# Kernel tuning notes

Measured on AMD Instinct MI355X. Metric: run time of the kernel, lower is better.

The kernel has to match this reference:

```python
import jax, jax.numpy as jnp
import numpy as np

EMBED = 50
SEQ = 100
NLABEL = 15
HID = 20
VOCAB = 50000
BATCH = 8192


def gru_scan(xs, W, U, b, return_sequences):
    """Keras GRUCell (reset_after=True, gate order z,r,h).
    xs: (B, T, D). W: (D, 3H), U: (H, 3H), b: (2, 3H) [input bias, recurrent bias].
    """
    B = xs.shape[0]
    H = U.shape[0]
    bi, br = b[0], b[1]
    h0 = jnp.zeros((B, H), dtype=xs.dtype)

    def step(h, x_t):
        mx = x_t @ W + bi                      # (B, 3H)
        mh = h @ U + br                        # (B, 3H)
        xz, xr, xh = mx[:, :H], mx[:, H:2*H], mx[:, 2*H:]
        hz, hr, hh_ = mh[:, :H], mh[:, H:2*H], mh[:, 2*H:]
        z = jax.nn.sigmoid(xz + hz)
        r = jax.nn.sigmoid(xr + hr)
        hh = jnp.tanh(xh + r * hh_)
        h_new = z * h + (1.0 - z) * hh
        return h_new, h_new

    xs_t = jnp.swapaxes(xs, 0, 1)              # (T, B, D)
    h_last, hs = jax.lax.scan(step, h0, xs_t)
    if return_sequences:
        return jnp.swapaxes(hs, 0, 1)          # (B, T, H)
    return h_last                               # (B, H)


def setup_inputs() -> dict:
    key = jax.random.key(0)
    ks = jax.random.split(key, 9)
    s = 0.05
    return {
        "x": jax.random.randint(ks[0], (BATCH, SEQ), 0, VOCAB),
        "emb_table": jax.random.normal(ks[1], (VOCAB, EMBED), jnp.float32) * s,
        "W1": jax.random.normal(ks[2], (EMBED, 3 * HID), jnp.float32) * s,
        "U1": jax.random.normal(ks[3], (HID, 3 * HID), jnp.float32) * s,
        "b1": jnp.zeros((2, 3 * HID), jnp.float32),
        "W2": jax.random.normal(ks[4], (HID, 3 * HID), jnp.float32) * s,
        "U2": jax.random.normal(ks[5], (HID, 3 * HID), jnp.float32) * s,
        "b2": jnp.zeros((2, 3 * HID), jnp.float32),
        "Wd": jax.random.normal(ks[6], (HID, NLABEL), jnp.float32) * s,
        "bd": jnp.zeros((NLABEL,), jnp.float32),
        "drop_rate": 0,
    }


def reference(x, emb_table, W1, U1, b1, W2, U2, b2, Wd, bd, drop_rate):
    emb = emb_table[x]                               # (B, T, E)
    seq = gru_scan(emb, W1, U1, b1, return_sequences=True)   # (B, T, H)
    enc = gru_scan(seq, W2, U2, b2, return_sequences=False)  # (B, H)
    # drop_rate == 0 -> tf.nn.dropout is identity
    logits = enc @ Wd + bd                           # (B, 15)
    return logits
```

## Files before the change

kernel.cpp:

```cpp
#include <hip/hip_runtime.h>
#include <hip/hip_bf16.h>
#include <hip/hip_fp16.h>

#define SEQ_T 100
#define HID 20
#define EMB_D 50
#define VOCAB_N 50000
#define TABW 60
#define NTILE 3125
#define BBLK 782

typedef short sh8 __attribute__((ext_vector_type(8)));
typedef float f4  __attribute__((ext_vector_type(4)));

#define OFF_U1P 0
#define OFF_W2P 600
#define OFF_U2P 1200
#define OFF_B1  3600
#define OFF_B2  3720
#define OFF_WD  3840
#define OFF_BD  4140
#define OFF_TAB 4160

__device__ __forceinline__ float ldf(const void* p, int i, int isf) {
  return isf ? ((const float*)p)[i]
             : __bfloat162float(((const __hip_bfloat16*)p)[i]);
}
__device__ __forceinline__ short f2bf(float f) {
  unsigned u = __float_as_uint(f);
  u += 0x7fffu + ((u >> 16) & 1u);
  return (short)(u >> 16);
}
__device__ __forceinline__ float rdl(float v, int l) {
  return __uint_as_float(__builtin_amdgcn_readlane(__float_as_uint(v), l));
}
__device__ __forceinline__ int detect_isf(const void* emb) {
  uint4 dv = ((const uint4*)emb)[threadIdx.x & 63];
  int big = 0;
#pragma unroll
  for (int i = 0; i < 4; ++i) {
    unsigned w = ((const unsigned*)&dv)[i];
    big |= (((w >> 7) & 0xFF) >= 140) | (((w >> 23) & 0xFF) >= 140);
  }
  return (__ballot(big) != 0ull) ? 1 : 0;
}

__global__ __launch_bounds__(256) void build_table(
    const void* __restrict__ emb, const void* __restrict__ W1,
    const void* __restrict__ b1,
    const void* __restrict__ U1, const void* __restrict__ W2,
    const void* __restrict__ U2, const void* __restrict__ b2,
    const void* __restrict__ Wd, const void* __restrict__ bd,
    float* __restrict__ ws)
{
  const int isf = detect_isf(emb);
  if (blockIdx.x == 0) {
    const int t = threadIdx.x;
    unsigned* wsu = (unsigned*)ws;
    for (int i = t; i < 600; i += 256) {
      const int j = i / 10, p = i % 10;
      const int k0 = 2 * p, k1 = 2 * p + 1;
#define PK(M) ((unsigned)__half_as_ushort(__float2half_rn(ldf(M, k0 * 60 + j, isf))) | \
               ((unsigned)__half_as_ushort(__float2half_rn(ldf(M, k1 * 60 + j, isf))) << 16))
      wsu[OFF_U1P + i] = PK(U1);
      wsu[OFF_W2P + i] = PK(W2);
      wsu[OFF_U2P + i] = PK(U2);
#undef PK
    }
    for (int i = t; i < 120; i += 256) {
      ws[OFF_B1 + i] = ldf(b1, i, isf);
      ws[OFF_B2 + i] = ldf(b2, i, isf);
    }
    for (int i = t; i < 300; i += 256) ws[OFF_WD + i] = ldf(Wd, i, isf);
    for (int i = t; i < 15;  i += 256) ws[OFF_BD + i] = ldf(bd, i, isf);
  }

  const int L = threadIdx.x & 63, q = L >> 4, c = L & 15;
  const int wid = blockIdx.x * 4 + (threadIdx.x >> 6);
  float* __restrict__ tab = ws + OFF_TAB;

  __shared__ int4 sB[64][8];
  if (threadIdx.x < 64) {
#pragma unroll
    for (int nt = 0; nt < 4; ++nt) {
      const int col = nt * 16 + c;
      sh8 B0, B1;
#pragma unroll
      for (int jj = 0; jj < 8; ++jj) {
        const int k0 = q * 8 + jj, k1 = 32 + q * 8 + jj;
        B0[jj] = (col < TABW) ? f2bf(ldf(W1, k0 * TABW + col, isf)) : (short)0;
        B1[jj] = (col < TABW && k1 < EMB_D)
                     ? f2bf(ldf(W1, k1 * TABW + col, isf)) : (short)0;
      }
      sB[L][nt * 2]     = *(const int4*)&B0;
      sB[L][nt * 2 + 1] = *(const int4*)&B1;
    }
  }
  float bi[4];
#pragma unroll
  for (int nt = 0; nt < 4; ++nt) {
    const int col = nt * 16 + c;
    bi[nt] = (col < TABW) ? ldf(b1, col, isf) : 0.f;
  }
  __syncthreads();

  for (int tile = wid; tile < NTILE; tile += BBLK * 4) {
    const int v0 = tile * 16;
    sh8 A0, A1;
#pragma unroll
    for (int jj = 0; jj < 8; ++jj) { A0[jj] = 0; A1[jj] = 0; }
    if (!isf) {
      const unsigned short* eb = (const unsigned short*)emb;
      const size_t rb = (size_t)(v0 + c) * EMB_D;
#pragma unroll
      for (int i = 0; i < 4; ++i) {
        unsigned d = *(const unsigned*)(eb + rb + q * 8 + 2 * i);
        A0[2 * i] = (short)(d & 0xffff); A0[2 * i + 1] = (short)(d >> 16);
      }
      const int k1b = 32 + q * 8;
#pragma unroll
      for (int i = 0; i < 4; ++i) {
        const int k = k1b + 2 * i;
        if (k + 1 < EMB_D) {
          unsigned d = *(const unsigned*)(eb + rb + k);
          A1[2 * i] = (short)(d & 0xffff); A1[2 * i + 1] = (short)(d >> 16);
        }
      }
    } else {
      const float* ef = (const float*)emb;
      const size_t rb = (size_t)(v0 + c) * EMB_D;
#pragma unroll
      for (int jj = 0; jj < 8; ++jj) {
        const int k0 = q * 8 + jj, k1 = 32 + q * 8 + jj;
        A0[jj] = f2bf(ef[rb + k0]);
        A1[jj] = (k1 < EMB_D) ? f2bf(ef[rb + k1]) : (short)0;
      }
    }
#pragma unroll
    for (int nt = 0; nt < 4; ++nt) {
      int4 b0i = sB[L][nt * 2], b1i = sB[L][nt * 2 + 1];
      sh8 B0 = *(const sh8*)&b0i, B1 = *(const sh8*)&b1i;
      const int col = nt * 16 + c;
      f4 acc = { bi[nt], bi[nt], bi[nt], bi[nt] };
      acc = __builtin_amdgcn_mfma_f32_16x16x32_bf16(A0, B0, acc, 0, 0, 0);
      acc = __builtin_amdgcn_mfma_f32_16x16x32_bf16(A1, B1, acc, 0, 0, 0);
      if (col < TABW) {
#pragma unroll
        for (int r = 0; r < 4; ++r)
          tab[(size_t)(v0 + q * 4 + r) * TABW + col] = acc[r];
      }
    }
  }
}

__global__ __launch_bounds__(256, 8) void gru_main(
    const int* __restrict__ x, const float* __restrict__ ws,
    const void* __restrict__ emb, void* __restrict__ out)
{
  const int isf = detect_isf(emb);
  const int j = threadIdx.x & 63;
  const int e = __builtin_amdgcn_readfirstlane(blockIdx.x * 4 + (threadIdx.x >> 6));
  const int jc = j < TABW ? j : 0;

  const int* xr = x + (size_t)e * SEQ_T;
  const float* tab = ws + OFF_TAB;
  const int o1 = jc * 40;
  const int jc4 = jc * 4;
  const int a1 = ((j - 20) & 63) * 4;
  const int a2 = ((j + 40) & 63) * 4;
  const float br1 = ws[OFF_B1 + 60 + jc];
  const float bi2 = ws[OFF_B2 + jc];
  const float br2 = ws[OFF_B2 + 60 + jc];
  float h2out;

  asm volatile(
    "global_load_dwordx4 v[10:13], %[o1], %[wsp] offset:0\n\t"
    "global_load_dwordx4 v[14:17], %[o1], %[wsp] offset:16\n\t"
    "global_load_dwordx2 v[18:19], %[o1], %[wsp] offset:32\n\t"
    "v_add_u32 v44, 0x960, %[o1]\n\t"
    "v_add_u32 v45, 0x12c0, %[o1]\n\t"
    "global_load_dwordx4 v[20:23], v44, %[wsp] offset:0\n\t"
    "global_load_dwordx4 v[24:27], v44, %[wsp] offset:16\n\t"
    "global_load_dwordx2 v[28:29], v44, %[wsp] offset:32\n\t"
    "global_load_dwordx4 v[30:33], v45, %[wsp] offset:0\n\t"
    "global_load_dwordx4 v[34:37], v45, %[wsp] offset:16\n\t"
    "global_load_dwordx2 v[38:39], v45, %[wsp] offset:32\n\t"
    "s_mov_b64 s[20:21], 0\n\ts_mov_b64 s[22:23], 0\n\t"
    "s_mov_b64 s[24:25], 0\n\ts_mov_b64 s[26:27], 0\n\t"
    "s_mov_b64 s[28:29], 0\n\t"
    "s_mov_b64 s[30:31], 0\n\ts_mov_b64 s[32:33], 0\n\t"
    "s_mov_b64 s[34:35], 0\n\ts_mov_b64 s[36:37], 0\n\t"
    "s_mov_b64 s[38:39], 0\n\t"
    "s_mov_b64 s[40:41], 0\n\ts_mov_b64 s[42:43], 0\n\t"
    "s_mov_b64 s[44:45], 0\n\ts_mov_b64 s[46:47], 0\n\t"
    "s_mov_b64 s[48:49], 0\n\t"
    "s_mov_b64 s[50:51], 0\n\ts_mov_b64 s[52:53], 0\n\t"
    "s_mov_b64 s[54:55], 0\n\ts_mov_b64 s[56:57], 0\n\t"
    "s_mov_b64 s[58:59], 0\n\t"
    "v_mov_b32 v40, 0\n\t"
    "v_mov_b32 v41, 0\n\t"
    "s_load_dword s65, %[xp], 0x0\n\t"
    "s_load_dword s66, %[xp], 0x4\n\t"
    "s_load_dword s68, %[xp], 0x8\n\t"
    "s_waitcnt lgkmcnt(0)\n\t"
    "s_mul_i32 s65, s65, 240\n\t"
    "s_mul_i32 s66, s66, 240\n\t"
    "s_mul_i32 s68, s68, 240\n\t"
    "v_add_u32 v50, s65, %[jc4]\n\t"
    "global_load_dword v53, v50, %[tabp]\n\t"
    "v_add_u32 v50, s66, %[jc4]\n\t"
    "global_load_dword v42, v50, %[tabp]\n\t"
    "v_add_u32 v50, s68, %[jc4]\n\t"
    "global_load_dword v43, v50, %[tabp]\n\t"
    "s_load_dword s65, %[xp], 0xc\n\t"
    "s_load_dword s68, %[xp], 0x10\n\t"
    "s_movk_i32 s64, 0x14\n\t"
    "s_movk_i32 s69, 0x18\n\t"
    "s_movk_i32 s67, 0x32\n\t"
    "s_waitcnt vmcnt(2)\n\t"
    "v_mov_b32 v44, %[br1]\n\t"
    "v_dot2_f32_f16 v44, s40, v10, v44\n\t"
    "v_dot2_f32_f16 v44, s41, v11, v44\n\t"
    "v_dot2_f32_f16 v44, s42, v12, v44\n\t"
    "v_dot2_f32_f16 v44, s43, v13, v44\n\t"
    "v_dot2_f32_f16 v44, s44, v14, v44\n\t"
    "v_dot2_f32_f16 v44, s45, v15, v44\n\t"
    "v_dot2_f32_f16 v44, s46, v16, v44\n\t"
    "v_dot2_f32_f16 v44, s47, v17, v44\n\t"
    "v_dot2_f32_f16 v44, s48, v18, v44\n\t"
    "v_dot2_f32_f16 v44, s49, v19, v44\n\t"
    "v_add_f32 v45, v53, v44\n\t"
    "v_mul_f32 v45, 0xbfb8aa3b, v45\n\t"
    "v_exp_f32 v45, v45\n\t"
    "s_nop 1\n\t"
    "v_add_f32 v45, 1.0, v45\n\t"
    "v_rcp_f32 v45, v45\n\t"
    "s_nop 1\n\t"
    "ds_bpermute_b32 v46, %[a1], v45\n\t"
    "s_waitcnt lgkmcnt(0)\n\t"
    "v_fma_f32 v47, v46, v44, v53\n\t"
    "v_mul_f32 v47, 0x4038aa3b, v47\n\t"
    "v_exp_f32 v47, v47\n\t"
    "s_nop 1\n\t"
    "v_add_f32 v47, 1.0, v47\n\t"
    "v_rcp_f32 v47, v47\n\t"
    "s_nop 1\n\t"
    "v_fma_f32 v47, -2.0, v47, 1.0\n\t"
    "ds_bpermute_b32 v46, %[a2], v47\n\t"
    "s_waitcnt lgkmcnt(0)\n\t"
    "v_sub_f32 v48, v40, v46\n\t"
    "v_fma_f32 v40, v45, v48, v46\n\t"
    "s_nop 1\n\t"
    "v_cvt_f16_f32 v46, v40\n\t"
    "s_nop 1\n\t"
    "ds_swizzle_b32 v47, v46 offset:0x041F\n\t"
    "s_waitcnt lgkmcnt(0)\n\t"
    "v_pack_b32_f16 v46, v46, v47\n\t"
    "s_nop 1\n\t"
    "v_readlane_b32 s20, v46, 0\n\t"
    "v_readlane_b32 s21, v46, 2\n\t"
    "v_readlane_b32 s22, v46, 4\n\t"
    "v_readlane_b32 s23, v46, 6\n\t"
    "v_readlane_b32 s24, v46, 8\n\t"
    "v_readlane_b32 s25, v46, 10\n\t"
    "v_readlane_b32 s26, v46, 12\n\t"
    "v_readlane_b32 s27, v46, 14\n\t"
    "v_readlane_b32 s28, v46, 16\n\t"
    "v_readlane_b32 s29, v46, 18\n\t"
    "0:\n\t"
    "v_mov_b32 v44, %[br1]\n\t"
    "v_mov_b32 v51, %[bi2]\n\t"
    "v_mov_b32 v52, %[br2]\n\t"
    "v_dot2_f32_f16 v44, s20, v10, v44\n\t"
    "v_dot2_f32_f16 v51, s20, v20, v51\n\t"
    "v_dot2_f32_f16 v52, s50, v30, v52\n\t"
    "v_dot2_f32_f16 v44, s21, v11, v44\n\t"
    "v_dot2_f32_f16 v51, s21, v21, v51\n\t"
    "v_dot2_f32_f16 v52, s51, v31, v52\n\t"
    "v_dot2_f32_f16 v44, s22, v12, v44\n\t"
    "v_dot2_f32_f16 v51, s22, v22, v51\n\t"
    "v_dot2_f32_f16 v52, s52, v32, v52\n\t"
    "v_dot2_f32_f16 v44, s23, v13, v44\n\t"
    "v_dot2_f32_f16 v51, s23, v23, v51\n\t"
    "v_dot2_f32_f16 v52, s53, v33, v52\n\t"
    "v_dot2_f32_f16 v44, s24, v14, v44\n\t"
    "v_dot2_f32_f16 v51, s24, v24, v51\n\t"
    "v_dot2_f32_f16 v52, s54, v34, v52\n\t"
    "v_dot2_f32_f16 v44, s25, v15, v44\n\t"
    "v_dot2_f32_f16 v51, s25, v25, v51\n\t"
    "v_dot2_f32_f16 v52, s55, v35, v52\n\t"
    "v_dot2_f32_f16 v44, s26, v16, v44\n\t"
    "v_dot2_f32_f16 v51, s26, v26, v51\n\t"
    "v_dot2_f32_f16 v52, s56, v36, v52\n\t"
    "v_dot2_f32_f16 v44, s27, v17, v44\n\t"
    "v_dot2_f32_f16 v51, s27, v27, v51\n\t"
    "v_dot2_f32_f16 v52, s57, v37, v52\n\t"
    "v_dot2_f32_f16 v44, s28, v18, v44\n\t"
    "v_dot2_f32_f16 v51, s28, v28, v51\n\t"
    "v_dot2_f32_f16 v52, s58, v38, v52\n\t"
    "v_dot2_f32_f16 v44, s29, v19, v44\n\t"
    "v_dot2_f32_f16 v51, s29, v29, v51\n\t"
    "v_dot2_f32_f16 v52, s59, v39, v52\n\t"
    "s_waitcnt vmcnt(1)\n\t"
    "v_add_f32 v45, v42, v44\n\t"
    "v_add_f32 v53, v51, v52\n\t"
    "v_mul_f32 v45, 0xbfb8aa3b, v45\n\t"
    "v_mul_f32 v53, 0xbfb8aa3b, v53\n\t"
    "v_exp_f32 v45, v45\n\t"
    "v_exp_f32 v53, v53\n\t"
    "v_add_f32 v45, 1.0, v45\n\t"
    "v_add_f32 v53, 1.0, v53\n\t"
    "v_rcp_f32 v45, v45\n\t"
    "v_rcp_f32 v53, v53\n\t"
    "ds_bpermute_b32 v46, %[a1], v45\n\t"
    "ds_bpermute_b32 v54, %[a1], v53\n\t"
    "s_mul_i32 s66, s65, 240\n\t"
    "v_add_u32 v50, s66, %[jc4]\n\t"
    "s_waitcnt lgkmcnt(0)\n\t"
    "v_fma_f32 v47, v46, v44, v42\n\t"
    "v_fma_f32 v55, v54, v52, v51\n\t"
    "global_load_dword v42, v50, %[tabp]\n\t"
    "v_mul_f32 v47, 0x4038aa3b, v47\n\t"
    "v_mul_f32 v55, 0x4038aa3b, v55\n\t"
    "v_exp_f32 v47, v47\n\t"
    "v_exp_f32 v55, v55\n\t"
    "v_add_f32 v47, 1.0, v47\n\t"
    "v_add_f32 v55, 1.0, v55\n\t"
    "v_rcp_f32 v47, v47\n\t"
    "v_rcp_f32 v55, v55\n\t"
    "v_fma_f32 v47, -2.0, v47, 1.0\n\t"
    "v_fma_f32 v55, -2.0, v55, 1.0\n\t"
    "ds_bpermute_b32 v46, %[a2], v47\n\t"
    "ds_bpermute_b32 v54, %[a2], v55\n\t"
    "s_waitcnt lgkmcnt(0)\n\t"
    "v_sub_f32 v48, v40, v46\n\t"
    "v_sub_f32 v51, v41, v54\n\t"
    "v_fma_f32 v40, v45, v48, v46\n\t"
    "v_fma_f32 v41, v53, v51, v54\n\t"
    "v_cvt_f16_f32 v46, v40\n\t"
    "v_cvt_f16_f32 v54, v41\n\t"
    "ds_swizzle_b32 v47, v46 offset:0x041F\n\t"
    "ds_swizzle_b32 v55, v54 offset:0x041F\n\t"
    "s_waitcnt lgkmcnt(0)\n\t"
    "v_pack_b32_f16 v46, v46, v47\n\t"
    "v_pack_b32_f16 v54, v54, v55\n\t"
    "s_min_u32 s64, s64, 396\n\t"
    "s_load_dword s65, %[xp], s64\n\t"
    "s_add_u32 s64, s64, 8\n\t"
    "s_nop 0\n\t"
    "v_readlane_b32 s40, v46, 0\n\t"
    "v_readlane_b32 s41, v46, 2\n\t"
    "v_readlane_b32 s42, v46, 4\n\t"
    "v_readlane_b32 s43, v46, 6\n\t"
    "v_readlane_b32 s44, v46, 8\n\t"
    "v_readlane_b32 s45, v46, 10\n\t"
    "v_readlane_b32 s46, v46, 12\n\t"
    "v_readlane_b32 s47, v46, 14\n\t"
    "v_readlane_b32 s48, v46, 16\n\t"
    "v_readlane_b32 s49, v46, 18\n\t"
    "v_readlane_b32 s30, v54, 0\n\t"
    "v_readlane_b32 s31, v54, 2\n\t"
    "v_readlane_b32 s32, v54, 4\n\t"
    "v_readlane_b32 s33, v54, 6\n\t"
    "v_readlane_b32 s34, v54, 8\n\t"
    "v_readlane_b32 s35, v54, 10\n\t"
    "v_readlane_b32 s36, v54, 12\n\t"
    "v_readlane_b32 s37, v54, 14\n\t"
    "v_readlane_b32 s38, v54, 16\n\t"
    "v_readlane_b32 s39, v54, 18\n\t"
    "v_mov_b32 v44, %[br1]\n\t"
    "v_mov_b32 v51, %[bi2]\n\t"
    "v_mov_b32 v52, %[br2]\n\t"
    "v_dot2_f32_f16 v44, s40, v10, v44\n\t"
    "v_dot2_f32_f16 v51, s40, v20, v51\n\t"
    "v_dot2_f32_f16 v52, s30, v30, v52\n\t"
    "v_dot2_f32_f16 v44, s41, v11, v44\n\t"
    "v_dot2_f32_f16 v51, s41, v21, v51\n\t"
    "v_dot2_f32_f16 v52, s31, v31, v52\n\t"
    "v_dot2_f32_f16 v44, s42, v12, v44\n\t"
    "v_dot2_f32_f16 v51, s42, v22, v51\n\t"
    "v_dot2_f32_f16 v52, s32, v32, v52\n\t"
    "v_dot2_f32_f16 v44, s43, v13, v44\n\t"
    "v_dot2_f32_f16 v51, s43, v23, v51\n\t"
    "v_dot2_f32_f16 v52, s33, v33, v52\n\t"
    "v_dot2_f32_f16 v44, s44, v14, v44\n\t"
    "v_dot2_f32_f16 v51, s44, v24, v51\n\t"
    "v_dot2_f32_f16 v52, s34, v34, v52\n\t"
    "v_dot2_f32_f16 v44, s45, v15, v44\n\t"
    "v_dot2_f32_f16 v51, s45, v25, v51\n\t"
    "v_dot2_f32_f16 v52, s35, v35, v52\n\t"
    "v_dot2_f32_f16 v44, s46, v16, v44\n\t"
    "v_dot2_f32_f16 v51, s46, v26, v51\n\t"
    "v_dot2_f32_f16 v52, s36, v36, v52\n\t"
    "v_dot2_f32_f16 v44, s47, v17, v44\n\t"
    "v_dot2_f32_f16 v51, s47, v27, v51\n\t"
    "v_dot2_f32_f16 v52, s37, v37, v52\n\t"
    "v_dot2_f32_f16 v44, s48, v18, v44\n\t"
    "v_dot2_f32_f16 v51, s48, v28, v51\n\t"
    "v_dot2_f32_f16 v52, s38, v38, v52\n\t"
    "v_dot2_f32_f16 v44, s49, v19, v44\n\t"
    "v_dot2_f32_f16 v51, s49, v29, v51\n\t"
    "v_dot2_f32_f16 v52, s39, v39, v52\n\t"
    "s_waitcnt vmcnt(1)\n\t"
    "v_add_f32 v45, v43, v44\n\t"
    "v_add_f32 v53, v51, v52\n\t"
    "v_mul_f32 v45, 0xbfb8aa3b, v45\n\t"
    "v_mul_f32 v53, 0xbfb8aa3b, v53\n\t"
    "v_exp_f32 v45, v45\n\t"
    "v_exp_f32 v53, v53\n\t"
    "v_add_f32 v45, 1.0, v45\n\t"
    "v_add_f32 v53, 1.0, v53\n\t"
    "v_rcp_f32 v45, v45\n\t"
    "v_rcp_f32 v53, v53\n\t"
    "ds_bpermute_b32 v46, %[a1], v45\n\t"
    "ds_bpermute_b32 v54, %[a1], v53\n\t"
    "s_mul_i32 s66, s68, 240\n\t"
    "v_add_u32 v50, s66, %[jc4]\n\t"
    "s_waitcnt lgkmcnt(0)\n\t"
    "v_fma_f32 v47, v46, v44, v43\n\t"
    "v_fma_f32 v55, v54, v52, v51\n\t"
    "global_load_dword v43, v50, %[tabp]\n\t"
    "v_mul_f32 v47, 0x4038aa3b, v47\n\t"
    "v_mul_f32 v55, 0x4038aa3b, v55\n\t"
    "v_exp_f32 v47, v47\n\t"
    "v_exp_f32 v55, v55\n\t"
    "v_add_f32 v47, 1.0, v47\n\t"
    "v_add_f32 v55, 1.0, v55\n\t"
    "v_rcp_f32 v47, v47\n\t"
    "v_rcp_f32 v55, v55\n\t"
    "v_fma_f32 v47, -2.0, v47, 1.0\n\t"
    "v_fma_f32 v55, -2.0, v55, 1.0\n\t"
    "ds_bpermute_b32 v46, %[a2], v47\n\t"
    "ds_bpermute_b32 v54, %[a2], v55\n\t"
    "s_waitcnt lgkmcnt(0)\n\t"
    "v_sub_f32 v48, v40, v46\n\t"
    "v_sub_f32 v51, v41, v54\n\t"
    "v_fma_f32 v40, v45, v48, v46\n\t"
    "v_fma_f32 v41, v53, v51, v54\n\t"
    "v_cvt_f16_f32 v46, v40\n\t"
    "v_cvt_f16_f32 v54, v41\n\t"
    "ds_swizzle_b32 v47, v46 offset:0x041F\n\t"
    "ds_swizzle_b32 v55, v54 offset:0x041F\n\t"
    "s_waitcnt lgkmcnt(0)\n\t"
    "v_pack_b32_f16 v46, v46, v47\n\t"
    "v_pack_b32_f16 v54, v54, v55\n\t"
    "s_min_u32 s69, s69, 392\n\t"
    "s_load_dword s68, %[xp], s69\n\t"
    "s_add_u32 s69, s69, 8\n\t"
    "s_nop 0\n\t"
    "v_readlane_b32 s20, v46, 0\n\t"
    "v_readlane_b32 s21, v46, 2\n\t"
    "v_readlane_b32 s22, v46, 4\n\t"
    "v_readlane_b32 s23, v46, 6\n\t"
    "v_readlane_b32 s24, v46, 8\n\t"
    "v_readlane_b32 s25, v46, 10\n\t"
    "v_readlane_b32 s26, v46, 12\n\t"
    "v_readlane_b32 s27, v46, 14\n\t"
    "v_readlane_b32 s28, v46, 16\n\t"
    "v_readlane_b32 s29, v46, 18\n\t"
    "v_readlane_b32 s50, v54, 0\n\t"
    "v_readlane_b32 s51, v54, 2\n\t"
    "v_readlane_b32 s52, v54, 4\n\t"
    "v_readlane_b32 s53, v54, 6\n\t"
    "v_readlane_b32 s54, v54, 8\n\t"
    "v_readlane_b32 s55, v54, 10\n\t"
    "v_readlane_b32 s56, v54, 12\n\t"
    "v_readlane_b32 s57, v54, 14\n\t"
    "v_readlane_b32 s58, v54, 16\n\t"
    "v_readlane_b32 s59, v54, 18\n\t"
    "s_sub_u32 s67, s67, 1\n\t"
    "s_cmp_lg_u32 s67, 0\n\t"
    "s_cbranch_scc1 0b\n\t"
    "s_waitcnt vmcnt(0) lgkmcnt(0)\n\t"
    "v_mov_b32 %[h2o], v41\n\t"
    : [h2o] "=v"(h2out)
    : [wsp] "s"(ws), [xp] "s"(xr), [tabp] "s"(tab),
      [o1] "v"(o1), [jc4] "v"(jc4), [a1] "v"(a1), [a2] "v"(a2),
      [br1] "v"(br1), [bi2] "v"(bi2), [br2] "v"(br2)
    : "memory", "vcc", "scc",
      "v10","v11","v12","v13","v14","v15","v16","v17","v18","v19",
      "v20","v21","v22","v23","v24","v25","v26","v27","v28","v29",
      "v30","v31","v32","v33","v34","v35","v36","v37","v38","v39",
      "v40","v41","v42","v43","v44","v45","v46","v47","v48","v49","v50",
      "v51","v52","v53","v54","v55",
      "s20","s21","s22","s23","s24","s25","s26","s27","s28","s29",
      "s30","s31","s32","s33","s34","s35","s36","s37","s38","s39",
      "s40","s41","s42","s43","s44","s45","s46","s47","s48","s49",
      "s50","s51","s52","s53","s54","s55","s56","s57","s58","s59",
      "s64","s65","s66","s67","s68","s69");

  if (j < 15) {
    float a = ws[OFF_BD + j];
#pragma unroll
    for (int k = 0; k < HID; ++k)
      a = fmaf(rdl(h2out, k), ws[OFF_WD + k * 15 + j], a);
    if (isf) ((float*)out)[(size_t)e * 15 + j] = a;
    else ((__hip_bfloat16*)out)[(size_t)e * 15 + j] = __float2bfloat16(a);
  }
}

extern "C" void kernel_launch(void* const* d_in, const int* in_sizes, int n_in,
                              void* d_out, int out_size, void* d_ws, size_t ws_size,
                              hipStream_t stream) {
  const int* x    = (const int*)d_in[0];
  const void* emb = d_in[1];
  const void* W1  = d_in[2];
  const void* U1  = d_in[3];
  const void* b1  = d_in[4];
  const void* W2  = d_in[5];
  const void* U2  = d_in[6];
  const void* b2  = d_in[7];
  const void* Wd  = d_in[8];
  const void* bd  = d_in[9];
  float* ws = (float*)d_ws;

  build_table<<<BBLK, 256, 0, stream>>>(
      emb, W1, b1, U1, W2, U2, b2, Wd, bd, ws);
  gru_main<<<2048, 256, 0, stream>>>(x, ws, emb, d_out);
}
```

Measured before the change: 232.7 us.

## Compute all gate columns per lane to replace LDS permutes with permlane swaps

Each lane now computes two gate columns (A and B) of the recurrent matrix-vector product, so the z/r product and the candidate activation sit in the same lane. This removes the ds_bpermute round trips from the per-step critical path. The remaining cross-half exchange uses v_permlane32_swap with a max-select, and the f16 pair swizzle becomes a DPP move. The cost is doubled dot-product and load work per step and many more VGPRs, with launch bounds lowered from 8 to 4 waves, which may reduce occupancy and latency hiding.

```diff
diff --git a/kernel.cpp b/kernel.cpp
--- a/kernel.cpp
+++ b/kernel.cpp
@@ -153,38 +153,54 @@
   }
 }
 
-__global__ __launch_bounds__(256, 8) void gru_main(
+__global__ __launch_bounds__(256, 4) void gru_main(
     const int* __restrict__ x, const float* __restrict__ ws,
     const void* __restrict__ emb, void* __restrict__ out)
 {
   const int isf = detect_isf(emb);
   const int j = threadIdx.x & 63;
   const int e = __builtin_amdgcn_readfirstlane(blockIdx.x * 4 + (threadIdx.x >> 6));
-  const int jc = j < TABW ? j : 0;
+
+  const int jcA = (j < 20) ? j : (j >= 32 && j < 52) ? j - 12 : 0;
+  const int jcB = (j >= 32 && j < 52) ? j + 8 : 40;
 
   const int* xr = x + (size_t)e * SEQ_T;
   const float* tab = ws + OFF_TAB;
-  const int o1 = jc * 40;
-  const int jc4 = jc * 4;
-  const int a1 = ((j - 20) & 63) * 4;
-  const int a2 = ((j + 40) & 63) * 4;
-  const float br1 = ws[OFF_B1 + 60 + jc];
-  const float bi2 = ws[OFF_B2 + jc];
-  const float br2 = ws[OFF_B2 + 60 + jc];
+  const int o1A = jcA * 40, o1B = jcB * 40;
+  const int jcA4 = jcA * 4, jcB4 = jcB * 4;
+  const float brA1 = ws[OFF_B1 + 60 + jcA];
+  const float brB1 = ws[OFF_B1 + 60 + jcB];
+  const float biA2 = ws[OFF_B2 + jcA];
+  const float biB2 = ws[OFF_B2 + jcB];
+  const float brA2 = ws[OFF_B2 + 60 + jcA];
+  const float brB2 = ws[OFF_B2 + 60 + jcB];
   float h2out;
 
   asm volatile(
-    "global_load_dwordx4 v[10:13], %[o1], %[wsp] offset:0\n\t"
-    "global_load_dwordx4 v[14:17], %[o1], %[wsp] offset:16\n\t"
-    "global_load_dwordx2 v[18:19], %[o1], %[wsp] offset:32\n\t"
-    "v_add_u32 v44, 0x960, %[o1]\n\t"
-    "v_add_u32 v45, 0x12c0, %[o1]\n\t"
+    "global_load_dwordx4 v[10:13], %[o1A], %[wsp] offset:0\n\t"
+    "global_load_dwordx4 v[14:17], %[o1A], %[wsp] offset:16\n\t"
+    "global_load_dwordx2 v[18:19], %[o1A], %[wsp] offset:32\n\t"
+    "v_add_u32 v44, 0x960, %[o1A]\n\t"
+    "v_add_u32 v45, 0x12c0, %[o1A]\n\t"
     "global_load_dwordx4 v[20:23], v44, %[wsp] offset:0\n\t"
     "global_load_dwordx4 v[24:27], v44, %[wsp] offset:16\n\t"
     "global_load_dwordx2 v[28:29], v44, %[wsp] offset:32\n\t"
     "global_load_dwordx4 v[30:33], v45, %[wsp] offset:0\n\t"
     "global_load_dwordx4 v[34:37], v45, %[wsp] offset:16\n\t"
     "global_load_dwordx2 v[38:39], v45, %[wsp] offset:32\n\t"
+    "global_load_dwordx4 v[60:63], %[o1B], %[wsp] offset:0\n\t"
+    "global_load_dwordx4 v[64:67], %[o1B], %[wsp] offset:16\n\t"
+    "global_load_dwordx2 v[68:69], %[o1B], %[wsp] offset:32\n\t"
+    "v_add_u32 v46, 0x960, %[o1B]\n\t"
+    "v_add_u32 v47, 0x12c0, %[o1B]\n\t"
+    "global_load_dwordx4 v[70:73], v46, %[wsp] offset:0\n\t"
+    "global_load_dwordx4 v[74:77], v46, %[wsp] offset:16\n\t"
+    "global_load_dwordx2 v[78:79], v46, %[wsp] offset:32\n\t"
+    "global_load_dwordx4 v[80:83], v47, %[wsp] offset:0\n\t"
+    "global_load_dwordx4 v[84:87], v47, %[wsp] offset:16\n\t"
+    "global_load_dwordx2 v[88:89], v47, %[wsp] offset:32\n\t"
+    "s_mov_b32 s60, 0\n\t"
+    "s_mov_b32 s61, 0xfffff\n\t"
     "s_mov_b64 s[20:21], 0\n\ts_mov_b64 s[22:23], 0\n\t"
     "s_mov_b64 s[24:25], 0\n\ts_mov_b64 s[26:27], 0\n\t"
     "s_mov_b64 s[28:29], 0\n\t"
@@ -206,29 +222,47 @@
     "s_mul_i32 s65, s65, 240\n\t"
     "s_mul_i32 s66, s66, 240\n\t"
     "s_mul_i32 s68, s68, 240\n\t"
-    "v_add_u32 v50, s65, %[jc4]\n\t"
+    "v_add_u32 v50, s65, %[jcA4]\n\t"
     "global_load_dword v53, v50, %[tabp]\n\t"
-    "v_add_u32 v50, s66, %[jc4]\n\t"
+    "v_add_u32 v50, s65, %[jcB4]\n\t"
+    "global_load_dword v55, v50, %[tabp]\n\t"
+    "v_add_u32 v50, s66, %[jcA4]\n\t"
     "global_load_dword v42, v50, %[tabp]\n\t"
-    "v_add_u32 v50, s68, %[jc4]\n\t"
+    "v_add_u32 v50, s66, %[jcB4]\n\t"
+    "global_load_dword v56, v50, %[tabp]\n\t"
+    "v_add_u32 v50, s68, %[jcA4]\n\t"
     "global_load_dword v43, v50, %[tabp]\n\t"
+    "v_add_u32 v50, s68, %[jcB4]\n\t"
+    "global_load_dword v57, v50, %[tabp]\n\t"
     "s_load_dword s65, %[xp], 0xc\n\t"
     "s_load_dword s68, %[xp], 0x10\n\t"
     "s_movk_i32 s64, 0x14\n\t"
     "s_movk_i32 s69, 0x18\n\t"
     "s_movk_i32 s67, 0x32\n\t"
-    "s_waitcnt vmcnt(2)\n\t"
-    "v_mov_b32 v44, %[br1]\n\t"
+    "s_waitcnt vmcnt(6)\n\t"
+    "v_mov_b32 v44, %[brA1]\n\t"
+    "v_mov_b32 v58, %[brB1]\n\t"
     "v_dot2_f32_f16 v44, s40, v10, v44\n\t"
+    "v_dot2_f32_f16 v58, s40, v60, v58\n\t"
     "v_dot2_f32_f16 v44, s41, v11, v44\n\t"
+    "v_dot2_f32_f16 v58, s41, v61, v58\n\t"
     "v_dot2_f32_f16 v44, s42, v12, v44\n\t"
+    "v_dot2_f32_f16 v58, s42, v62, v58\n\t"
     "v_dot2_f32_f16 v44, s43, v13, v44\n\t"
+    "v_dot2_f32_f16 v58, s43, v63, v58\n\t"
     "v_dot2_f32_f16 v44, s44, v14, v44\n\t"
+    "v_dot2_f32_f16 v58, s44, v64, v58\n\t"
     "v_dot2_f32_f16 v44, s45, v15, v44\n\t"
+    "v_dot2_f32_f16 v58, s45, v65, v58\n\t"
     "v_dot2_f32_f16 v44, s46, v16, v44\n\t"
+    "v_dot2_f32_f16 v58, s46, v66, v58\n\t"
     "v_dot2_f32_f16 v44, s47, v17, v44\n\t"
+    "v_dot2_f32_f16 v58, s47, v67, v58\n\t"
     "v_dot2_f32_f16 v44, s48, v18, v44\n\t"
+    "v_dot2_f32_f16 v58, s48, v68, v58\n\t"
     "v_dot2_f32_f16 v44, s49, v19, v44\n\t"
+    "v_dot2_f32_f16 v58, s49, v69, v58\n\t"
+    "s_waitcnt vmcnt(4)\n\t"
     "v_add_f32 v45, v53, v44\n\t"
     "v_mul_f32 v45, 0xbfb8aa3b, v45\n\t"
     "v_exp_f32 v45, v45\n\t"
@@ -236,9 +270,7 @@
     "v_add_f32 v45, 1.0, v45\n\t"
     "v_rcp_f32 v45, v45\n\t"
     "s_nop 1\n\t"
-    "ds_bpermute_b32 v46, %[a1], v45\n\t"
-    "s_waitcnt lgkmcnt(0)\n\t"
-    "v_fma_f32 v47, v46, v44, v53\n\t"
+    "v_fma_f32 v47, v45, v58, v55\n\t"
     "v_mul_f32 v47, 0x4038aa3b, v47\n\t"
     "v_exp_f32 v47, v47\n\t"
     "s_nop 1\n\t"
@@ -246,16 +278,19 @@
     "v_rcp_f32 v47, v47\n\t"
     "s_nop 1\n\t"
     "v_fma_f32 v47, -2.0, v47, 1.0\n\t"
-    "ds_bpermute_b32 v46, %[a2], v47\n\t"
-    "s_waitcnt lgkmcnt(0)\n\t"
+    "v_cndmask_b32 v47, -4.0, v47, s[60:61]\n\t"
+    "v_mov_b32 v48, v47\n\t"
+    "s_nop 1\n\t"
+    "v_permlane32_swap_b32 v47, v48\n\t"
+    "s_nop 1\n\t"
+    "v_max_f32 v46, v47, v48\n\t"
     "v_sub_f32 v48, v40, v46\n\t"
     "v_fma_f32 v40, v45, v48, v46\n\t"
-    "s_nop 1\n\t"
     "v_cvt_f16_f32 v46, v40\n\t"
     "s_nop 1\n\t"
-    "ds_swizzle_b32 v47, v46 offset:0x041F\n\t"
-    "s_waitcnt lgkmcnt(0)\n\t"
-    "v_pack_b32_f16 v46, v46, v47\n\t"
+    "v_mov_b32_dpp v48, v46 quad_perm:[1,0,3,2] row_mask:0xf bank_mask:0xf\n\t"
+    "s_nop 1\n\t"
+    "v_pack_b32_f16 v46, v46, v48\n\t"
     "s_nop 1\n\t"
     "v_readlane_b32 s20, v46, 0\n\t"
     "v_readlane_b32 s21, v46, 2\n\t"
@@ -268,40 +303,73 @@
     "v_readlane_b32 s28, v46, 16\n\t"
     "v_readlane_b32 s29, v46, 18\n\t"
     "0:\n\t"
-    "v_mov_b32 v44, %[br1]\n\t"
-    "v_mov_b32 v51, %[bi2]\n\t"
-    "v_mov_b32 v52, %[br2]\n\t"
+    "v_mov_b32 v44, %[brA1]\n\t"
+    "v_mov_b32 v58, %[brB1]\n\t"
+    "v_mov_b32 v51, %[biA2]\n\t"
+    "v_mov_b32 v54, %[biB2]\n\t"
+    "v_mov_b32 v52, %[brA2]\n\t"
+    "v_mov_b32 v55, %[brB2]\n\t"
     "v_dot2_f32_f16 v44, s20, v10, v44\n\t"
     "v_dot2_f32_f16 v51, s20, v20, v51\n\t"
     "v_dot2_f32_f16 v52, s50, v30, v52\n\t"
+    "v_dot2_f32_f16 v58, s20, v60, v58\n\t"
+    "v_dot2_f32_f16 v54, s20, v70, v54\n\t"
+    "v_dot2_f32_f16 v55, s50, v80, v55\n\t"
     "v_dot2_f32_f16 v44, s21, v11, v44\n\t"
     "v_dot2_f32_f16 v51, s21, v21, v51\n\t"
     "v_dot2_f32_f16 v52, s51, v31, v52\n\t"
+    "v_dot2_f32_f16 v58, s21, v61, v58\n\t"
+    "v_dot2_f32_f16 v54, s21, v71, v54\n\t"
+    "v_dot2_f32_f16 v55, s51, v81, v55\n\t"
     "v_dot2_f32_f16 v44, s22, v12, v44\n\t"
     "v_dot2_f32_f16 v51, s22, v22, v51\n\t"
     "v_dot2_f32_f16 v52, s52, v32, v52\n\t"
+    "v_dot2_f32_f16 v58, s22, v62, v58\n\t"
+    "v_dot2_f32_f16 v54, s22, v72, v54\n\t"
+    "v_dot2_f32_f16 v55, s52, v82, v55\n\t"
     "v_dot2_f32_f16 v44, s23, v13, v44\n\t"
     "v_dot2_f32_f16 v51, s23, v23, v51\n\t"
     "v_dot2_f32_f16 v52, s53, v33, v52\n\t"
+    "v_dot2_f32_f16 v58, s23, v63, v58\n\t"
+    "v_dot2_f32_f16 v54, s23, v73, v54\n\t"
+    "v_dot2_f32_f16 v55, s53, v83, v55\n\t"
     "v_dot2_f32_f16 v44, s24, v14, v44\n\t"
     "v_dot2_f32_f16 v51, s24, v24, v51\n\t"
     "v_dot2_f32_f16 v52, s54, v34, v52\n\t"
+    "v_dot2_f32_f16 v58, s24, v64, v58\n\t"
+    "v_dot2_f32_f16 v54, s24, v74, v54\n\t"
+    "v_dot2_f32_f16 v55, s54, v84, v55\n\t"
     "v_dot2_f32_f16 v44, s25, v15, v44\n\t"
     "v_dot2_f32_f16 v51, s25, v25, v51\n\t"
     "v_dot2_f32_f16 v52, s55, v35, v52\n\t"
+    "v_dot2_f32_f16 v58, s25, v65, v58\n\t"
+    "v_dot2_f32_f16 v54, s25, v75, v54\n\t"
+    "v_dot2_f32_f16 v55, s55, v85, v55\n\t"
     "v_dot2_f32_f16 v44, s26, v16, v44\n\t"
     "v_dot2_f32_f16 v51, s26, v26, v51\n\t"
     "v_dot2_f32_f16 v52, s56, v36, v52\n\t"
+    "v_dot2_f32_f16 v58, s26, v66, v58\n\t"
+    "v_dot2_f32_f16 v54, s26, v76, v54\n\t"
+    "v_dot2_f32_f16 v55, s56, v86, v55\n\t"
     "v_dot2_f32_f16 v44, s27, v17, v44\n\t"
     "v_dot2_f32_f16 v51, s27, v27, v51\n\t"
     "v_dot2_f32_f16 v52, s57, v37, v52\n\t"
+    "v_dot2_f32_f16 v58, s27, v67, v58\n\t"
+    "v_dot2_f32_f16 v54, s27, v77, v54\n\t"
+    "v_dot2_f32_f16 v55, s57, v87, v55\n\t"
     "v_dot2_f32_f16 v44, s28, v18, v44\n\t"
     "v_dot2_f32_f16 v51, s28, v28, v51\n\t"
     "v_dot2_f32_f16 v52, s58, v38, v52\n\t"
+    "v_dot2_f32_f16 v58, s28, v68, v58\n\t"
+    "v_dot2_f32_f16 v54, s28, v78, v54\n\t"
+    "v_dot2_f32_f16 v55, s58, v88, v55\n\t"
     "v_dot2_f32_f16 v44, s29, v19, v44\n\t"
     "v_dot2_f32_f16 v51, s29, v29, v51\n\t"
     "v_dot2_f32_f16 v52, s59, v39, v52\n\t"
-    "s_waitcnt vmcnt(1)\n\t"
+    "v_dot2_f32_f16 v58, s29, v69, v58\n\t"
+    "v_dot2_f32_f16 v54, s29, v79, v54\n\t"
+    "v_dot2_f32_f16 v55, s59, v89, v55\n\t"
+    "s_waitcnt vmcnt(2)\n\t"
     "v_add_f32 v45, v42, v44\n\t"
     "v_add_f32 v53, v51, v52\n\t"
     "v_mul_f32 v45, 0xbfb8aa3b, v45\n\t"
@@ -312,42 +380,52 @@
     "v_add_f32 v53, 1.0, v53\n\t"
     "v_rcp_f32 v45, v45\n\t"
     "v_rcp_f32 v53, v53\n\t"
-    "ds_bpermute_b32 v46, %[a1], v45\n\t"
-    "ds_bpermute_b32 v54, %[a1], v53\n\t"
+    "s_nop 0\n\t"
+    "v_fma_f32 v47, v45, v58, v56\n\t"
+    "v_fma_f32 v49, v53, v55, v54\n\t"
+    "s_waitcnt lgkmcnt(0)\n\t"
     "s_mul_i32 s66, s65, 240\n\t"
-    "v_add_u32 v50, s66, %[jc4]\n\t"
-    "s_waitcnt lgkmcnt(0)\n\t"
-    "v_fma_f32 v47, v46, v44, v42\n\t"
-    "v_fma_f32 v55, v54, v52, v51\n\t"
+    "v_add_u32 v50, s66, %[jcA4]\n\t"
     "global_load_dword v42, v50, %[tabp]\n\t"
-    "v_mul_f32 v47, 0x4038aa3b, v47\n\t"
-    "v_mul_f32 v55, 0x4038aa3b, v55\n\t"
-    "v_exp_f32 v47, v47\n\t"
-    "v_exp_f32 v55, v55\n\t"
-    "v_add_f32 v47, 1.0, v47\n\t"
-    "v_add_f32 v55, 1.0, v55\n\t"
-    "v_rcp_f32 v47, v47\n\t"
-    "v_rcp_f32 v55, v55\n\t"
-    "v_fma_f32 v47, -2.0, v47, 1.0\n\t"
-    "v_fma_f32 v55, -2.0, v55, 1.0\n\t"
-    "ds_bpermute_b32 v46, %[a2], v47\n\t"
-    "ds_bpermute_b32 v54, %[a2], v55\n\t"
-    "s_waitcnt lgkmcnt(0)\n\t"
-    "v_sub_f32 v48, v40, v46\n\t"
-    "v_sub_f32 v51, v41, v54\n\t"
-    "v_fma_f32 v40, v45, v48, v46\n\t"
-    "v_fma_f32 v41, v53, v51, v54\n\t"
-    "v_cvt_f16_f32 v46, v40\n\t"
-    "v_cvt_f16_f32 v54, v41\n\t"
-    "ds_swizzle_b32 v47, v46 offset:0x041F\n\t"
-    "ds_swizzle_b32 v55, v54 offset:0x041F\n\t"
-    "s_waitcnt lgkmcnt(0)\n\t"
-    "v_pack_b32_f16 v46, v46, v47\n\t"
-    "v_pack_b32_f16 v54, v54, v55\n\t"
+    "v_add_u32 v50, s66, %[jcB4]\n\t"
+    "global_load_dword v56, v50, %[tabp]\n\t"
     "s_min_u32 s64, s64, 396\n\t"
     "s_load_dword s65, %[xp], s64\n\t"
     "s_add_u32 s64, s64, 8\n\t"
+    "v_mul_f32 v47, 0x4038aa3b, v47\n\t"
+    "v_mul_f32 v49, 0x4038aa3b, v49\n\t"
+    "v_exp_f32 v47, v47\n\t"
+    "v_exp_f32 v49, v49\n\t"
+    "v_add_f32 v47, 1.0, v47\n\t"
+    "v_add_f32 v49, 1.0, v49\n\t"
+    "v_rcp_f32 v47, v47\n\t"
+    "v_rcp_f32 v49, v49\n\t"
     "s_nop 0\n\t"
+    "v_fma_f32 v47, -2.0, v47, 1.0\n\t"
+    "v_fma_f32 v49, -2.0, v49, 1.0\n\t"
+    "v_cndmask_b32 v47, -4.0, v47, s[60:61]\n\t"
+    "v_cndmask_b32 v49, -4.0, v49, s[60:61]\n\t"
+    "v_mov_b32 v48, v47\n\t"
+    "v_mov_b32 v59, v49\n\t"
+    "s_nop 1\n\t"
+    "v_permlane32_swap_b32 v47, v48\n\t"
+    "v_permlane32_swap_b32 v49, v59\n\t"
+    "s_nop 1\n\t"
+    "v_max_f32 v46, v47, v48\n\t"
+    "v_max_f32 v59, v49, v59\n\t"
+    "v_sub_f32 v48, v40, v46\n\t"
+    "v_fma_f32 v40, v45, v48, v46\n\t"
+    "v_sub_f32 v48, v41, v59\n\t"
+    "v_fma_f32 v41, v53, v48, v59\n\t"
+    "v_cvt_f16_f32 v46, v40\n\t"
+    "v_cvt_f16_f32 v47, v41\n\t"
+    "s_nop 1\n\t"
+    "v_mov_b32_dpp v48, v46 quad_perm:[1,0,3,2] row_mask:0xf bank_mask:0xf\n\t"
+    "v_mov_b32_dpp v49, v47 quad_perm:[1,0,3,2] row_mask:0xf bank_mask:0xf\n\t"
+    "s_nop 1\n\t"
+    "v_pack_b32_f16 v46, v46, v48\n\t"
+    "v_pack_b32_f16 v47, v47, v49\n\t"
+    "s_nop 1\n\t"
     "v_readlane_b32 s40, v46, 0\n\t"
     "v_readlane_b32 s41, v46, 2\n\t"
     "v_readlane_b32 s42, v46, 4\n\t"
@@ -358,50 +436,83 @@
     "v_readlane_b32 s47, v46, 14\n\t"
     "v_readlane_b32 s48, v46, 16\n\t"
     "v_readlane_b32 s49, v46, 18\n\t"
-    "v_readlane_b32 s30, v54, 0\n\t"
-    "v_readlane_b32 s31, v54, 2\n\t"
-    "v_readlane_b32 s32, v54, 4\n\t"
-    "v_readlane_b32 s33, v54, 6\n\t"
-    "v_readlane_b32 s34, v54, 8\n\t"
-    "v_readlane_b32 s35, v54, 10\n\t"
-    "v_readlane_b32 s36, v54, 12\n\t"
-    "v_readlane_b32 s37, v54, 14\n\t"
-    "v_readlane_b32 s38, v54, 16\n\t"
-    "v_readlane_b32 s39, v54, 18\n\t"
-    "v_mov_b32 v44, %[br1]\n\t"
-    "v_mov_b32 v51, %[bi2]\n\t"
-    "v_mov_b32 v52, %[br2]\n\t"
+    "v_readlane_b32 s30, v47, 0\n\t"
+    "v_readlane_b32 s31, v47, 2\n\t"
+    "v_readlane_b32 s32, v47, 4\n\t"
+    "v_readlane_b32 s33, v47, 6\n\t"
+    "v_readlane_b32 s34, v47, 8\n\t"
+    "v_readlane_b32 s35, v47, 10\n\t"
+    "v_readlane_b32 s36, v47, 12\n\t"
+    "v_readlane_b32 s37, v47, 14\n\t"
+    "v_readlane_b32 s38, v47, 16\n\t"
+    "v_readlane_b32 s39, v47, 18\n\t"
+    "v_mov_b32 v44, %[brA1]\n\t"
+    "v_mov_b32 v58, %[brB1]\n\t"
+    "v_mov_b32 v51, %[biA2]\n\t"
+    "v_mov_b32 v54, %[biB2]\n\t"
+    "v_mov_b32 v52, %[brA2]\n\t"
+    "v_mov_b32 v55, %[brB2]\n\t"
     "v_dot2_f32_f16 v44, s40, v10, v44\n\t"
     "v_dot2_f32_f16 v51, s40, v20, v51\n\t"
     "v_dot2_f32_f16 v52, s30, v30, v52\n\t"
+    "v_dot2_f32_f16 v58, s40, v60, v58\n\t"
+    "v_dot2_f32_f16 v54, s40, v70, v54\n\t"
+    "v_dot2_f32_f16 v55, s30, v80, v55\n\t"
     "v_dot2_f32_f16 v44, s41, v11, v44\n\t"
     "v_dot2_f32_f16 v51, s41, v21, v51\n\t"
     "v_dot2_f32_f16 v52, s31, v31, v52\n\t"
+    "v_dot2_f32_f16 v58, s41, v61, v58\n\t"
+    "v_dot2_f32_f16 v54, s41, v71, v54\n\t"
+    "v_dot2_f32_f16 v55, s31, v81, v55\n\t"
     "v_dot2_f32_f16 v44, s42, v12, v44\n\t"
     "v_dot2_f32_f16 v51, s42, v22, v51\n\t"
     "v_dot2_f32_f16 v52, s32, v32, v52\n\t"
+    "v_dot2_f32_f16 v58, s42, v62, v58\n\t"
+    "v_dot2_f32_f16 v54, s42, v72, v54\n\t"
+    "v_dot2_f32_f16 v55, s32, v82, v55\n\t"
     "v_dot2_f32_f16 v44, s43, v13, v44\n\t"
     "v_dot2_f32_f16 v51, s43, v23, v51\n\t"
     "v_dot2_f32_f16 v52, s33, v33, v52\n\t"
+    "v_dot2_f32_f16 v58, s43, v63, v58\n\t"
+    "v_dot2_f32_f16 v54, s43, v73, v54\n\t"
+    "v_dot2_f32_f16 v55, s33, v83, v55\n\t"
     "v_dot2_f32_f16 v44, s44, v14, v44\n\t"
     "v_dot2_f32_f16 v51, s44, v24, v51\n\t"
     "v_dot2_f32_f16 v52, s34, v34, v52\n\t"
+    "v_dot2_f32_f16 v58, s44, v64, v58\n\t"
+    "v_dot2_f32_f16 v54, s44, v74, v54\n\t"
+    "v_dot2_f32_f16 v55, s34, v84, v55\n\t"
     "v_dot2_f32_f16 v44, s45, v15, v44\n\t"
     "v_dot2_f32_f16 v51, s45, v25, v51\n\t"
     "v_dot2_f32_f16 v52, s35, v35, v52\n\t"
+    "v_dot2_f32_f16 v58, s45, v65, v58\n\t"
+    "v_dot2_f32_f16 v54, s45, v75, v54\n\t"
+    "v_dot2_f32_f16 v55, s35, v85, v55\n\t"
     "v_dot2_f32_f16 v44, s46, v16, v44\n\t"
     "v_dot2_f32_f16 v51, s46, v26, v51\n\t"
     "v_dot2_f32_f16 v52, s36, v36, v52\n\t"
+    "v_dot2_f32_f16 v58, s46, v66, v58\n\t"
+    "v_dot2_f32_f16 v54, s46, v76, v54\n\t"
+    "v_dot2_f32_f16 v55, s36, v86, v55\n\t"
     "v_dot2_f32_f16 v44, s47, v17, v44\n\t"
     "v_dot2_f32_f16 v51, s47, v27, v51\n\t"
     "v_dot2_f32_f16 v52, s37, v37, v52\n\t"
+    "v_dot2_f32_f16 v58, s47, v67, v58\n\t"
+    "v_dot2_f32_f16 v54, s47, v77, v54\n\t"
+    "v_dot2_f32_f16 v55, s37, v87, v55\n\t"
     "v_dot2_f32_f16 v44, s48, v18, v44\n\t"
     "v_dot2_f32_f16 v51, s48, v28, v51\n\t"
     "v_dot2_f32_f16 v52, s38, v38, v52\n\t"
+    "v_dot2_f32_f16 v58, s48, v68, v58\n\t"
+    "v_dot2_f32_f16 v54, s48, v78, v54\n\t"
+    "v_dot2_f32_f16 v55, s38, v88, v55\n\t"
     "v_dot2_f32_f16 v44, s49, v19, v44\n\t"
     "v_dot2_f32_f16 v51, s49, v29, v51\n\t"
     "v_dot2_f32_f16 v52, s39, v39, v52\n\t"
-    "s_waitcnt vmcnt(1)\n\t"
+    "v_dot2_f32_f16 v58, s49, v69, v58\n\t"
+    "v_dot2_f32_f16 v54, s49, v79, v54\n\t"
+    "v_dot2_f32_f16 v55, s39, v89, v55\n\t"
+    "s_waitcnt vmcnt(2)\n\t"
     "v_add_f32 v45, v43, v44\n\t"
     "v_add_f32 v53, v51, v52\n\t"
     "v_mul_f32 v45, 0xbfb8aa3b, v45\n\t"
@@ -412,42 +523,52 @@
     "v_add_f32 v53, 1.0, v53\n\t"
     "v_rcp_f32 v45, v45\n\t"
     "v_rcp_f32 v53, v53\n\t"
-    "ds_bpermute_b32 v46, %[a1], v45\n\t"
-    "ds_bpermute_b32 v54, %[a1], v53\n\t"
+    "s_nop 0\n\t"
+    "v_fma_f32 v47, v45, v58, v57\n\t"
+    "v_fma_f32 v49, v53, v55, v54\n\t"
+    "s_waitcnt lgkmcnt(0)\n\t"
     "s_mul_i32 s66, s68, 240\n\t"
-    "v_add_u32 v50, s66, %[jc4]\n\t"
-    "s_waitcnt lgkmcnt(0)\n\t"
-    "v_fma_f32 v47, v46, v44, v43\n\t"
-    "v_fma_f32 v55, v54, v52, v51\n\t"
+    "v_add_u32 v50, s66, %[jcA4]\n\t"
     "global_load_dword v43, v50, %[tabp]\n\t"
-    "v_mul_f32 v47, 0x4038aa3b, v47\n\t"
-    "v_mul_f32 v55, 0x4038aa3b, v55\n\t"
-    "v_exp_f32 v47, v47\n\t"
-    "v_exp_f32 v55, v55\n\t"
-    "v_add_f32 v47, 1.0, v47\n\t"
-    "v_add_f32 v55, 1.0, v55\n\t"
-    "v_rcp_f32 v47, v47\n\t"
-    "v_rcp_f32 v55, v55\n\t"
-    "v_fma_f32 v47, -2.0, v47, 1.0\n\t"
-    "v_fma_f32 v55, -2.0, v55, 1.0\n\t"
-    "ds_bpermute_b32 v46, %[a2], v47\n\t"
-    "ds_bpermute_b32 v54, %[a2], v55\n\t"
-    "s_waitcnt lgkmcnt(0)\n\t"
-    "v_sub_f32 v48, v40, v46\n\t"
-    "v_sub_f32 v51, v41, v54\n\t"
-    "v_fma_f32 v40, v45, v48, v46\n\t"
-    "v_fma_f32 v41, v53, v51, v54\n\t"
-    "v_cvt_f16_f32 v46, v40\n\t"
-    "v_cvt_f16_f32 v54, v41\n\t"
-    "ds_swizzle_b32 v47, v46 offset:0x041F\n\t"
-    "ds_swizzle_b32 v55, v54 offset:0x041F\n\t"
-    "s_waitcnt lgkmcnt(0)\n\t"
-    "v_pack_b32_f16 v46, v46, v47\n\t"
-    "v_pack_b32_f16 v54, v54, v55\n\t"
+    "v_add_u32 v50, s66, %[jcB4]\n\t"
+    "global_load_dword v57, v50, %[tabp]\n\t"
     "s_min_u32 s69, s69, 392\n\t"
     "s_load_dword s68, %[xp], s69\n\t"
     "s_add_u32 s69, s69, 8\n\t"
+    "v_mul_f32 v47, 0x4038aa3b, v47\n\t"
+    "v_mul_f32 v49, 0x4038aa3b, v49\n\t"
+    "v_exp_f32 v47, v47\n\t"
+    "v_exp_f32 v49, v49\n\t"
+    "v_add_f32 v47, 1.0, v47\n\t"
+    "v_add_f32 v49, 1.0, v49\n\t"
+    "v_rcp_f32 v47, v47\n\t"
+    "v_rcp_f32 v49, v49\n\t"
     "s_nop 0\n\t"
+    "v_fma_f32 v47, -2.0, v47, 1.0\n\t"
+    "v_fma_f32 v49, -2.0, v49, 1.0\n\t"
+    "v_cndmask_b32 v47, -4.0, v47, s[60:61]\n\t"
+    "v_cndmask_b32 v49, -4.0, v49, s[60:61]\n\t"
+    "v_mov_b32 v48, v47\n\t"
+    "v_mov_b32 v59, v49\n\t"
+    "s_nop 1\n\t"
+    "v_permlane32_swap_b32 v47, v48\n\t"
+    "v_permlane32_swap_b32 v49, v59\n\t"
+    "s_nop 1\n\t"
+    "v_max_f32 v46, v47, v48\n\t"
+    "v_max_f32 v59, v49, v59\n\t"
+    "v_sub_f32 v48, v40, v46\n\t"
+    "v_fma_f32 v40, v45, v48, v46\n\t"
+    "v_sub_f32 v48, v41, v59\n\t"
+    "v_fma_f32 v41, v53, v48, v59\n\t"
+    "v_cvt_f16_f32 v46, v40\n\t"
+    "v_cvt_f16_f32 v47, v41\n\t"
+    "s_nop 1\n\t"
+    "v_mov_b32_dpp v48, v46 quad_perm:[1,0,3,2] row_mask:0xf bank_mask:0xf\n\t"
+    "v_mov_b32_dpp v49, v47 quad_perm:[1,0,3,2] row_mask:0xf bank_mask:0xf\n\t"
+    "s_nop 1\n\t"
+    "v_pack_b32_f16 v46, v46, v48\n\t"
+    "v_pack_b32_f16 v47, v47, v49\n\t"
+    "s_nop 1\n\t"
     "v_readlane_b32 s20, v46, 0\n\t"
     "v_readlane_b32 s21, v46, 2\n\t"
     "v_readlane_b32 s22, v46, 4\n\t"
@@ -458,16 +579,16 @@
     "v_readlane_b32 s27, v46, 14\n\t"
     "v_readlane_b32 s28, v46, 16\n\t"
     "v_readlane_b32 s29, v46, 18\n\t"
-    "v_readlane_b32 s50, v54, 0\n\t"
-    "v_readlane_b32 s51, v54, 2\n\t"
-    "v_readlane_b32 s52, v54, 4\n\t"
-    "v_readlane_b32 s53, v54, 6\n\t"
-    "v_readlane_b32 s54, v54, 8\n\t"
-    "v_readlane_b32 s55, v54, 10\n\t"
-    "v_readlane_b32 s56, v54, 12\n\t"
-    "v_readlane_b32 s57, v54, 14\n\t"
-    "v_readlane_b32 s58, v54, 16\n\t"
-    "v_readlane_b32 s59, v54, 18\n\t"
+    "v_readlane_b32 s50, v47, 0\n\t"
+    "v_readlane_b32 s51, v47, 2\n\t"
+    "v_readlane_b32 s52, v47, 4\n\t"
+    "v_readlane_b32 s53, v47, 6\n\t"
+    "v_readlane_b32 s54, v47, 8\n\t"
+    "v_readlane_b32 s55, v47, 10\n\t"
+    "v_readlane_b32 s56, v47, 12\n\t"
+    "v_readlane_b32 s57, v47, 14\n\t"
+    "v_readlane_b32 s58, v47, 16\n\t"
+    "v_readlane_b32 s59, v47, 18\n\t"
     "s_sub_u32 s67, s67, 1\n\t"
     "s_cmp_lg_u32 s67, 0\n\t"
     "s_cbranch_scc1 0b\n\t"
@@ -475,19 +596,23 @@
     "v_mov_b32 %[h2o], v41\n\t"
     : [h2o] "=v"(h2out)
     : [wsp] "s"(ws), [xp] "s"(xr), [tabp] "s"(tab),
-      [o1] "v"(o1), [jc4] "v"(jc4), [a1] "v"(a1), [a2] "v"(a2),
-      [br1] "v"(br1), [bi2] "v"(bi2), [br2] "v"(br2)
+      [o1A] "v"(o1A), [o1B] "v"(o1B), [jcA4] "v"(jcA4), [jcB4] "v"(jcB4),
+      [brA1] "v"(brA1), [brB1] "v"(brB1), [biA2] "v"(biA2),
+      [biB2] "v"(biB2), [brA2] "v"(brA2), [brB2] "v"(brB2)
     : "memory", "vcc", "scc",
       "v10","v11","v12","v13","v14","v15","v16","v17","v18","v19",
       "v20","v21","v22","v23","v24","v25","v26","v27","v28","v29",
       "v30","v31","v32","v33","v34","v35","v36","v37","v38","v39",
       "v40","v41","v42","v43","v44","v45","v46","v47","v48","v49","v50",
-      "v51","v52","v53","v54","v55",
+      "v51","v52","v53","v54","v55","v56","v57","v58","v59",
+      "v60","v61","v62","v63","v64","v65","v66","v67","v68","v69",
+      "v70","v71","v72","v73","v74","v75","v76","v77","v78","v79",
+      "v80","v81","v82","v83","v84","v85","v86","v87","v88","v89",
       "s20","s21","s22","s23","s24","s25","s26","s27","s28","s29",
       "s30","s31","s32","s33","s34","s35","s36","s37","s38","s39",
       "s40","s41","s42","s43","s44","s45","s46","s47","s48","s49",
       "s50","s51","s52","s53","s54","s55","s56","s57","s58","s59",
-      "s64","s65","s66","s67","s68","s69");
+      "s60","s61","s64","s65","s66","s67","s68","s69");
 
   if (j < 15) {
     float a = ws[OFF_BD + j];
```

After: 290.1 us. 24.6% more time.
